# Kernel tuning notes

Measured on AMD Instinct MI355X. Metric: run time of the kernel, lower is better.

## Reference

```python
import jax, jax.numpy as jnp
import numpy as np

B, D, N = 2, 512, 2048
H, MQ, MV = 8, 64, 64
SCALE = 1.0 / np.sqrt(D).astype(np.float32)  # 1/sqrt(num_dim_q), full dim


def setup_inputs() -> dict:
    key = jax.random.key(0)
    ks = jax.random.split(key, 9)
    s = 0.02
    return {
        "Q": jax.random.normal(ks[0], (B, D, N), jnp.float32),
        "Wq": jax.random.normal(ks[1], (MQ * H, D), jnp.float32) * s,
        "bq": jnp.zeros((MQ * H,), jnp.float32),
        "Wk": jax.random.normal(ks[2], (MQ * H, D), jnp.float32) * s,
        "bk": jnp.zeros((MQ * H,), jnp.float32),
        "Wv": jax.random.normal(ks[3], (MV * H, D), jnp.float32) * s,
        "bv": jnp.zeros((MV * H,), jnp.float32),
        "Wo": jax.random.normal(ks[4], (D, MV * H), jnp.float32) * s,
        "bo": jnp.zeros((D,), jnp.float32),
    }


def _conv1x1(x, W, b):
    # Conv1d with kernel_size=1 == per-position linear: [B,Cin,N] -> [B,Cout,N]
    return jnp.einsum("bcn,oc->bon", x, W) + b[None, :, None]


def reference(Q, Wq, bq, Wk, bk, Wv, bv, Wo, bo):
    q = _conv1x1(Q, Wq, bq)  # [B, MQ*H, N]
    k = _conv1x1(Q, Wk, bk)
    v = _conv1x1(Q, Wv, bv)  # [B, MV*H, N]
    b = Q.shape[0]
    n = Q.shape[2]
    # channel index factors as (dim, head): channel = d*H + h (matches torch .view)
    q = q.reshape(b, MQ, H, n)
    k = k.reshape(b, MQ, H, n)
    v = v.reshape(b, MV, H, n)
    scores = jnp.einsum("bdhq,bdhk->bhqk", q, k) * SCALE  # [B,H,Nq,Nk]
    attn = jax.nn.softmax(scores, axis=-1)
    o = jnp.einsum("bhqk,bdhk->bdhq", attn, v)  # [B, MV, H, Nq]
    o = o.reshape(b, MV * H, n)
    return _conv1x1(o, Wo, bo)  # [B, D, N]
```

## Files before the change

kernel.cpp:

```cpp
#include <hip/hip_runtime.h>

#define DEV __device__ __forceinline__

typedef __bf16 bf16;
typedef __bf16 bf16x8 __attribute__((ext_vector_type(8)));
typedef __bf16 bf16x4 __attribute__((ext_vector_type(4)));
typedef float f32x4 __attribute__((ext_vector_type(4)));

#define B_ 2
#define D_ 512
#define N_ 2048
#define H_ 8
#define MD_ 64
#define SCALE_F (0.04419417382415922f * 1.4426950408889634f)

DEV void gload_lds16(const void* g, void* l) {
  __builtin_amdgcn_global_load_lds(
      (const __attribute__((address_space(1))) void*)g,
      (__attribute__((address_space(3))) void*)l, 16, 0, 0);
}

DEV f32x4 mfma16(bf16x8 a, bf16x8 b, f32x4 c) {
  return __builtin_amdgcn_mfma_f32_16x16x32_bf16(a, b, c, 0, 0, 0);
}

__global__ __launch_bounds__(256) void prep_w(
    const float* __restrict__ Wq, const float* __restrict__ bq,
    const float* __restrict__ Wk, const float* __restrict__ bk,
    const float* __restrict__ Wv, const float* __restrict__ bv,
    const float* __restrict__ Wo,
    bf16* __restrict__ Wf, float* __restrict__ biasf, bf16* __restrict__ Wor) {
  int row = blockIdx.x;
  int t = threadIdx.x;
  if (row < 1536) {
    const float* src;
    float scale = 1.0f;
    if (row < 512)       { src = Wq + (size_t)row * 512; scale = SCALE_F; }
    else if (row < 1024) { src = Wk + (size_t)(row - 512) * 512; }
    else                 { src = Wv + (size_t)(row - 1024) * 512; }
    for (int c = t; c < 512; c += 256)
      Wf[(size_t)row * 512 + c] = (bf16)(src[c] * scale);
    if (t == 0) {
      float bb;
      if (row < 512)       bb = bq[row] * SCALE_F;
      else if (row < 1024) bb = bk[row - 512];
      else                 bb = bv[row - 1024];
      biasf[row] = bb;
    }
  } else {
    int r = row - 1536;
    for (int c2 = t; c2 < 512; c2 += 256) {
      int hh = c2 >> 6, dd = c2 & 63;
      Wor[(size_t)r * 512 + c2] = (bf16)Wo[(size_t)r * 512 + dd * 8 + hh];
    }
  }
}

__global__ __launch_bounds__(256) void prep_qt(const float* __restrict__ Q,
                                               bf16* __restrict__ Qt) {
  __shared__ float tile[64][65];
  int b = blockIdx.z;
  int d0 = blockIdx.y * 64;
  int n0 = blockIdx.x * 64;
  int t = threadIdx.x;
  int r = t >> 2, cw = t & 3;

  const float* src = Q + ((size_t)(b * 512 + d0 + r)) * 2048 + n0 + cw * 16;
#pragma unroll
  for (int e4 = 0; e4 < 4; ++e4) {
    float4 v = *(const float4*)(src + e4 * 4);
    tile[r][cw * 16 + e4 * 4 + 0] = v.x;
    tile[r][cw * 16 + e4 * 4 + 1] = v.y;
    tile[r][cw * 16 + e4 * 4 + 2] = v.z;
    tile[r][cw * 16 + e4 * 4 + 3] = v.w;
  }
  __syncthreads();
  bf16x8 o0{}, o1{};
#pragma unroll
  for (int e = 0; e < 8; ++e) {
    o0[e] = (bf16)tile[cw * 16 + e][r];
    o1[e] = (bf16)tile[cw * 16 + 8 + e][r];
  }
  bf16* dst = Qt + ((size_t)(b * 2048 + n0 + r)) * 512 + d0 + cw * 16;
  *(bf16x8*)dst = o0;
  *((bf16x8*)dst + 1) = o1;
}

__global__ __launch_bounds__(256) void qkv_gemm(
    const bf16* __restrict__ Wf, const bf16* __restrict__ Qt,
    const float* __restrict__ biasf,
    bf16* __restrict__ qp, bf16* __restrict__ kp, bf16* __restrict__ vn) {
  __shared__ bf16 Al[128 * 32];
  __shared__ bf16 Bl[64 * 32];
  int b = blockIdx.z;
  int c0 = blockIdx.x * 128;
  int p0 = blockIdx.y * 64;
  int tid = threadIdx.x, w = tid >> 6, lane = tid & 63;
  int wm = w >> 1, wn = w & 1;
  int g = lane >> 4, l15 = lane & 15;

  const bf16* Abase = Wf + (size_t)c0 * 512;
  const bf16* Bbase = Qt + ((size_t)b * 2048 + p0) * 512;

  f32x4 acc[4][2] = {};

  for (int ks = 0; ks < 16; ++ks) {
    int k0 = ks * 32;
    __syncthreads();
#pragma unroll
    for (int i = 0; i < 2; ++i) {
      int rowl = w * 32 + i * 16 + (lane >> 2);
      gload_lds16(Abase + (size_t)rowl * 512 + k0 + (lane & 3) * 8,
                  Al + (w * 32 + i * 16) * 32);
    }
    {
      int browl = w * 16 + (lane >> 2);
      gload_lds16(Bbase + (size_t)browl * 512 + k0 + (lane & 3) * 8,
                  Bl + w * 16 * 32);
    }
    __syncthreads();
    bf16x8 a[4], bb[2];
#pragma unroll
    for (int mi = 0; mi < 4; ++mi)
      a[mi] = *(const bf16x8*)(Al + (wm * 64 + mi * 16 + l15) * 32 + g * 8);
#pragma unroll
    for (int ni = 0; ni < 2; ++ni)
      bb[ni] = *(const bf16x8*)(Bl + (wn * 32 + ni * 16 + l15) * 32 + g * 8);
#pragma unroll
    for (int mi = 0; mi < 4; ++mi)
#pragma unroll
      for (int ni = 0; ni < 2; ++ni)
        acc[mi][ni] = mfma16(a[mi], bb[ni], acc[mi][ni]);
  }

#pragma unroll
  for (int mi = 0; mi < 4; ++mi) {
#pragma unroll
    for (int ni = 0; ni < 2; ++ni) {
#pragma unroll
      for (int r = 0; r < 4; ++r) {
        int row = c0 + wm * 64 + mi * 16 + g * 4 + r;
        int p = p0 + wn * 32 + ni * 16 + l15;
        float val = acc[mi][ni][r] + biasf[row];
        bf16 hv = (bf16)val;
        if (row < 512) {
          int c = row;
          qp[(((size_t)b * 8 + (c & 7)) * 2048 + p) * 64 + (c >> 3)] = hv;
        } else if (row < 1024) {
          int c = row - 512;
          kp[(((size_t)b * 8 + (c & 7)) * 2048 + p) * 64 + (c >> 3)] = hv;
        } else {
          int c = row - 1024;
          vn[((size_t)b * 512 + c) * 2048 + p] = hv;
        }
      }
    }
  }
}

__global__ __launch_bounds__(512) void attn_k(
    const bf16* __restrict__ qp, const bf16* __restrict__ kp,
    const bf16* __restrict__ vn, bf16* __restrict__ Op,
    float* __restrict__ mbuf, float* __restrict__ lbuf) {
  __shared__ bf16 Ks[2][64 * 64];
  __shared__ bf16 Vs[2][64 * 64];
  __shared__ bf16 Ps[128 * 64];
  int q0 = blockIdx.x * 128;
  int bh = blockIdx.y;
  int z = blockIdx.z;
  int b = bh >> 3, h = bh & 7;
  int tid = threadIdx.x, w = tid >> 6, lane = tid & 63;
  int g = lane >> 4, l15 = lane & 15;
  int irow = w * 16 + l15;

  bf16x8 qreg[2];
#pragma unroll
  for (int ks2 = 0; ks2 < 2; ++ks2)
    qreg[ks2] = *(const bf16x8*)(qp + ((size_t)bh * 2048 + q0 + irow) * 64 +
                                 ks2 * 32 + g * 8);

  int krow = tid >> 3;
  int kch = (tid & 7) ^ (krow & 7);

  const bf16* Kall = kp + (size_t)bh * 2048 * 64 + (size_t)z * 16 * 64 * 64;
  const bf16* Vall = vn + ((size_t)(b * 512 + h)) * 2048 + (size_t)z * 16 * 64;

  gload_lds16(Kall + (size_t)krow * 64 + kch * 8, Ks[0] + w * 512);
  gload_lds16(Vall + (size_t)krow * 16384 + kch * 8, Vs[0] + w * 512);

  f32x4 oacc[4] = {};
  float mrow = -1e30f, rs = 0.0f;

  __syncthreads();

  for (int t = 0; t < 16; ++t) {
    int cur = t & 1, nxt = cur ^ 1;
    int tn = (t < 15) ? t + 1 : 15;

    gload_lds16(Kall + (size_t)tn * 64 * 64 + (size_t)krow * 64 + kch * 8,
                Ks[nxt] + w * 512);
    gload_lds16(Vall + (size_t)tn * 64 + (size_t)krow * 16384 + kch * 8,
                Vs[nxt] + w * 512);

    f32x4 st[4] = {};
    __builtin_amdgcn_s_setprio(1);
#pragma unroll
    for (int ks2 = 0; ks2 < 2; ++ks2) {
#pragma unroll
      for (int jt = 0; jt < 4; ++jt) {
        int jrow = jt * 16 + l15;
        bf16x8 kb = *(const bf16x8*)(Ks[cur] + jrow * 64 + (((ks2 * 4 + g) ^ (jrow & 7)) << 3));
        st[jt] = mfma16(kb, qreg[ks2], st[jt]);
      }
    }
    __builtin_amdgcn_s_setprio(0);

    float rm = st[0][0];
#pragma unroll
    for (int jt = 0; jt < 4; ++jt)
#pragma unroll
      for (int i = 0; i < 4; ++i) rm = fmaxf(rm, st[jt][i]);
    rm = fmaxf(rm, __shfl_xor(rm, 16));
    rm = fmaxf(rm, __shfl_xor(rm, 32));

    if (__any(rm > mrow + 8.0f)) {
      float nm = fmaxf(mrow, rm);
      float esc = __builtin_amdgcn_exp2f(mrow - nm);
      mrow = nm;
      rs *= esc;
#pragma unroll
      for (int r = 0; r < 4; ++r) {
        float er = __shfl(esc, g * 4 + r, 64);
#pragma unroll
        for (int dt = 0; dt < 4; ++dt) oacc[dt][r] *= er;
      }
    }

#pragma unroll
    for (int jt = 0; jt < 4; ++jt) {
      bf16x4 pk;
#pragma unroll
      for (int i = 0; i < 4; ++i) {
        float pv = __builtin_amdgcn_exp2f(st[jt][i] - mrow);
        rs += pv;
        pk[i] = (bf16)pv;
      }
      int j0 = jt * 16 + g * 4;
      *(bf16x4*)(Ps + irow * 64 + (j0 ^ ((irow & 7) << 3))) = pk;
    }

    __builtin_amdgcn_s_setprio(1);
#pragma unroll
    for (int ks2 = 0; ks2 < 2; ++ks2) {
      bf16x8 pa = *(const bf16x8*)(Ps + irow * 64 + (((ks2 * 4 + g) ^ (irow & 7)) << 3));
#pragma unroll
      for (int dt = 0; dt < 4; ++dt) {
        int drow = dt * 16 + l15;
        bf16x8 vb = *(const bf16x8*)(Vs[cur] + drow * 64 + (((ks2 * 4 + g) ^ (drow & 7)) << 3));
        oacc[dt] = mfma16(pa, vb, oacc[dt]);
      }
    }
    __builtin_amdgcn_s_setprio(0);

    __syncthreads();
  }

  rs += __shfl_xor(rs, 16);
  rs += __shfl_xor(rs, 32);

  size_t zoff = (size_t)z * 16 * 2048;
#pragma unroll
  for (int dt = 0; dt < 4; ++dt) {
#pragma unroll
    for (int r = 0; r < 4; ++r) {
      int i = w * 16 + g * 4 + r;
      Op[(zoff + (size_t)bh * 2048 + q0 + i) * 64 + dt * 16 + l15] =
          (bf16)oacc[dt][r];
    }
  }
  if (lane < 16) {
    mbuf[zoff + (size_t)bh * 2048 + q0 + w * 16 + l15] = mrow;
    lbuf[zoff + (size_t)bh * 2048 + q0 + w * 16 + l15] = rs;
  }
}

__global__ __launch_bounds__(256) void combine(
    const bf16* __restrict__ Op, const float* __restrict__ mbuf,
    const float* __restrict__ lbuf, bf16* __restrict__ oh) {
  int idx = blockIdx.x * 256 + threadIdx.x;
  int row = idx >> 2;
  int dc = (idx & 3) * 16;
  float m0 = mbuf[row], m1 = mbuf[32768 + row];
  float l0 = lbuf[row], l1 = lbuf[32768 + row];
  float M = fmaxf(m0, m1);
  float w0 = __builtin_amdgcn_exp2f(m0 - M);
  float w1 = __builtin_amdgcn_exp2f(m1 - M);
  float invL = 1.0f / (w0 * l0 + w1 * l1);
  float a0 = w0 * invL, a1 = w1 * invL;

  const bf16x8* p0 = (const bf16x8*)(Op + (size_t)row * 64 + dc);
  const bf16x8* p1 = (const bf16x8*)(Op + (size_t)32768 * 64 + (size_t)row * 64 + dc);
  bf16x8* po = (bf16x8*)(oh + (size_t)row * 64 + dc);
#pragma unroll
  for (int v = 0; v < 2; ++v) {
    bf16x8 x0 = p0[v], x1 = p1[v];
    bf16x8 o;
#pragma unroll
    for (int e = 0; e < 8; ++e)
      o[e] = (bf16)(a0 * (float)x0[e] + a1 * (float)x1[e]);
    po[v] = o;
  }
}

__global__ __launch_bounds__(256) void out_gemm(
    const bf16* __restrict__ Wor, const bf16* __restrict__ oh,
    const float* __restrict__ bo, float* __restrict__ out) {
  __shared__ bf16 Al[128 * 32];
  __shared__ bf16 Bl[64 * 32];
  int b = blockIdx.z;
  int r0 = blockIdx.x * 128;
  int p0 = blockIdx.y * 64;
  int tid = threadIdx.x, w = tid >> 6, lane = tid & 63;
  int wm = w >> 1, wn = w & 1;
  int g = lane >> 4, l15 = lane & 15;

  const bf16* Abase = Wor + (size_t)r0 * 512;

  f32x4 acc[4][2] = {};

  for (int ks = 0; ks < 16; ++ks) {
    int k0 = ks * 32;
    int hh = k0 >> 6, d0 = k0 & 63;
    const bf16* Bbase = oh + (((size_t)b * 8 + hh) * 2048 + p0) * 64 + d0;
    __syncthreads();
#pragma unroll
    for (int i = 0; i < 2; ++i) {
      int rowl = w * 32 + i * 16 + (lane >> 2);
      gload_lds16(Abase + (size_t)rowl * 512 + k0 + (lane & 3) * 8,
                  Al + (w * 32 + i * 16) * 32);
    }
    {
      int browl = w * 16 + (lane >> 2);
      gload_lds16(Bbase + (size_t)browl * 64 + (lane & 3) * 8,
                  Bl + w * 16 * 32);
    }
    __syncthreads();
    bf16x8 a[4], bb[2];
#pragma unroll
    for (int mi = 0; mi < 4; ++mi)
      a[mi] = *(const bf16x8*)(Al + (wm * 64 + mi * 16 + l15) * 32 + g * 8);
#pragma unroll
    for (int ni = 0; ni < 2; ++ni)
      bb[ni] = *(const bf16x8*)(Bl + (wn * 32 + ni * 16 + l15) * 32 + g * 8);
#pragma unroll
    for (int mi = 0; mi < 4; ++mi)
#pragma unroll
      for (int ni = 0; ni < 2; ++ni)
        acc[mi][ni] = mfma16(a[mi], bb[ni], acc[mi][ni]);
  }

#pragma unroll
  for (int mi = 0; mi < 4; ++mi) {
#pragma unroll
    for (int ni = 0; ni < 2; ++ni) {
#pragma unroll
      for (int r = 0; r < 4; ++r) {
        int row = r0 + wm * 64 + mi * 16 + g * 4 + r;
        int p = p0 + wn * 32 + ni * 16 + l15;
        out[((size_t)b * 512 + row) * 2048 + p] = acc[mi][ni][r] + bo[row];
      }
    }
  }
}

extern "C" void kernel_launch(void* const* d_in, const int* in_sizes, int n_in,
                              void* d_out, int out_size, void* d_ws, size_t ws_size,
                              hipStream_t stream) {
  (void)in_sizes; (void)n_in; (void)out_size; (void)ws_size;
  const float* Q  = (const float*)d_in[0];
  const float* Wq = (const float*)d_in[1];
  const float* bq = (const float*)d_in[2];
  const float* Wk = (const float*)d_in[3];
  const float* bk = (const float*)d_in[4];
  const float* Wv = (const float*)d_in[5];
  const float* bv = (const float*)d_in[6];
  const float* Wo = (const float*)d_in[7];
  const float* bo = (const float*)d_in[8];
  float* out = (float*)d_out;

  char* ws = (char*)d_ws;
  bf16*  Wf    = (bf16*)(ws + 0);
  bf16*  Wor   = (bf16*)(ws + 1572864);
  float* biasf = (float*)(ws + 2097152);
  bf16*  Qt    = (bf16*)(ws + 2103296);
  bf16*  qp    = (bf16*)(ws + 6297600);
  bf16*  kp    = (bf16*)(ws + 10491904);
  bf16*  vn    = (bf16*)(ws + 14686208);
  bf16*  oh    = (bf16*)(ws + 18880512);
  bf16*  Opart = (bf16*)(ws + 23074816);
  float* mbuf  = (float*)(ws + 31463424);
  float* lbuf  = (float*)(ws + 31725568);

  prep_w<<<dim3(2048), dim3(256), 0, stream>>>(Wq, bq, Wk, bk, Wv, bv, Wo,
                                               Wf, biasf, Wor);
  prep_qt<<<dim3(32, 8, 2), dim3(256), 0, stream>>>(Q, Qt);
  qkv_gemm<<<dim3(12, 32, 2), dim3(256), 0, stream>>>(Wf, Qt, biasf, qp, kp, vn);
  attn_k<<<dim3(16, 16, 2), dim3(512), 0, stream>>>(qp, kp, vn, Opart, mbuf, lbuf);
  combine<<<dim3(512), dim3(256), 0, stream>>>(Opart, mbuf, lbuf, oh);
  out_gemm<<<dim3(4, 32, 2), dim3(256), 0, stream>>>(Wor, oh, bo, out);
}
```

Baseline: 81.92 us.

## Double-buffer GEMM LDS tiles and give each attention wave two query row groups

The QKV and output projection GEMMs now keep two LDS buffers. The next K-slice is issued before the MFMAs on the current slice, which removes one barrier per iteration and overlaps global loads with compute. The attention kernel drops from 512 to 256 threads, and each wave handles 32 query rows as two 16-row groups. Each K/V fragment read from LDS is then reused for two MFMAs, at the cost of more registers per thread and half as many waves per block. LDS use per GEMM block doubles.

```diff
diff --git a/kernel.cpp b/kernel.cpp
--- a/kernel.cpp
+++ b/kernel.cpp
@@ -90,8 +90,8 @@
     const bf16* __restrict__ Wf, const bf16* __restrict__ Qt,
     const float* __restrict__ biasf,
     bf16* __restrict__ qp, bf16* __restrict__ kp, bf16* __restrict__ vn) {
-  __shared__ bf16 Al[128 * 32];
-  __shared__ bf16 Bl[64 * 32];
+  __shared__ bf16 Al[2][128 * 32];
+  __shared__ bf16 Bl[2][64 * 32];
   int b = blockIdx.z;
   int c0 = blockIdx.x * 128;
   int p0 = blockIdx.y * 64;
@@ -102,35 +102,43 @@
   const bf16* Abase = Wf + (size_t)c0 * 512;
   const bf16* Bbase = Qt + ((size_t)b * 2048 + p0) * 512;
 
+  int arow0 = lane >> 2;
+  int ach = lane & 3;
+
   f32x4 acc[4][2] = {};
 
+#pragma unroll
+  for (int i = 0; i < 2; ++i)
+    gload_lds16(Abase + (size_t)(w * 32 + i * 16 + arow0) * 512 + ach * 8,
+                Al[0] + (w * 32 + i * 16) * 32);
+  gload_lds16(Bbase + (size_t)(w * 16 + arow0) * 512 + ach * 8,
+              Bl[0] + w * 16 * 32);
+  __syncthreads();
+
   for (int ks = 0; ks < 16; ++ks) {
-    int k0 = ks * 32;
-    __syncthreads();
-#pragma unroll
-    for (int i = 0; i < 2; ++i) {
-      int rowl = w * 32 + i * 16 + (lane >> 2);
-      gload_lds16(Abase + (size_t)rowl * 512 + k0 + (lane & 3) * 8,
-                  Al + (w * 32 + i * 16) * 32);
-    }
-    {
-      int browl = w * 16 + (lane >> 2);
-      gload_lds16(Bbase + (size_t)browl * 512 + k0 + (lane & 3) * 8,
-                  Bl + w * 16 * 32);
-    }
-    __syncthreads();
+    int cur = ks & 1, nxt = cur ^ 1;
+    if (ks < 15) {
+      int k0 = (ks + 1) * 32;
+#pragma unroll
+      for (int i = 0; i < 2; ++i)
+        gload_lds16(Abase + (size_t)(w * 32 + i * 16 + arow0) * 512 + k0 + ach * 8,
+                    Al[nxt] + (w * 32 + i * 16) * 32);
+      gload_lds16(Bbase + (size_t)(w * 16 + arow0) * 512 + k0 + ach * 8,
+                  Bl[nxt] + w * 16 * 32);
+    }
     bf16x8 a[4], bb[2];
 #pragma unroll
     for (int mi = 0; mi < 4; ++mi)
-      a[mi] = *(const bf16x8*)(Al + (wm * 64 + mi * 16 + l15) * 32 + g * 8);
+      a[mi] = *(const bf16x8*)(Al[cur] + (wm * 64 + mi * 16 + l15) * 32 + g * 8);
 #pragma unroll
     for (int ni = 0; ni < 2; ++ni)
-      bb[ni] = *(const bf16x8*)(Bl + (wn * 32 + ni * 16 + l15) * 32 + g * 8);
+      bb[ni] = *(const bf16x8*)(Bl[cur] + (wn * 32 + ni * 16 + l15) * 32 + g * 8);
 #pragma unroll
     for (int mi = 0; mi < 4; ++mi)
 #pragma unroll
       for (int ni = 0; ni < 2; ++ni)
         acc[mi][ni] = mfma16(a[mi], bb[ni], acc[mi][ni]);
+    __syncthreads();
   }
 
 #pragma unroll
@@ -158,7 +166,7 @@
   }
 }
 
-__global__ __launch_bounds__(512) void attn_k(
+__global__ __launch_bounds__(256) void attn_k(
     const bf16* __restrict__ qp, const bf16* __restrict__ kp,
     const bf16* __restrict__ vn, bf16* __restrict__ Op,
     float* __restrict__ mbuf, float* __restrict__ lbuf) {
@@ -171,25 +179,32 @@
   int b = bh >> 3, h = bh & 7;
   int tid = threadIdx.x, w = tid >> 6, lane = tid & 63;
   int g = lane >> 4, l15 = lane & 15;
-  int irow = w * 16 + l15;
-
-  bf16x8 qreg[2];
-#pragma unroll
-  for (int ks2 = 0; ks2 < 2; ++ks2)
-    qreg[ks2] = *(const bf16x8*)(qp + ((size_t)bh * 2048 + q0 + irow) * 64 +
-                                 ks2 * 32 + g * 8);
+
+  bf16x8 qreg[2][2];
+#pragma unroll
+  for (int rg = 0; rg < 2; ++rg)
+#pragma unroll
+    for (int ks2 = 0; ks2 < 2; ++ks2)
+      qreg[rg][ks2] = *(const bf16x8*)(
+          qp + ((size_t)bh * 2048 + q0 + w * 32 + rg * 16 + l15) * 64 +
+          ks2 * 32 + g * 8);
 
   int krow = tid >> 3;
-  int kch = (tid & 7) ^ (krow & 7);
+  int kch = tid & 7;
 
   const bf16* Kall = kp + (size_t)bh * 2048 * 64 + (size_t)z * 16 * 64 * 64;
   const bf16* Vall = vn + ((size_t)(b * 512 + h)) * 2048 + (size_t)z * 16 * 64;
 
-  gload_lds16(Kall + (size_t)krow * 64 + kch * 8, Ks[0] + w * 512);
-  gload_lds16(Vall + (size_t)krow * 16384 + kch * 8, Vs[0] + w * 512);
-
-  f32x4 oacc[4] = {};
-  float mrow = -1e30f, rs = 0.0f;
+#pragma unroll
+  for (int i = 0; i < 2; ++i) {
+    int row = krow + i * 32;
+    int ch = kch ^ (row & 7);
+    gload_lds16(Kall + (size_t)row * 64 + ch * 8, Ks[0] + (w * 8 + i * 32) * 64);
+    gload_lds16(Vall + (size_t)row * 16384 + ch * 8, Vs[0] + (w * 8 + i * 32) * 64);
+  }
+
+  f32x4 oacc[2][4] = {};
+  float mrow[2] = {-1e30f, -1e30f}, rs[2] = {0.0f, 0.0f};
 
   __syncthreads();
 
@@ -197,67 +212,92 @@
     int cur = t & 1, nxt = cur ^ 1;
     int tn = (t < 15) ? t + 1 : 15;
 
-    gload_lds16(Kall + (size_t)tn * 64 * 64 + (size_t)krow * 64 + kch * 8,
-                Ks[nxt] + w * 512);
-    gload_lds16(Vall + (size_t)tn * 64 + (size_t)krow * 16384 + kch * 8,
-                Vs[nxt] + w * 512);
-
-    f32x4 st[4] = {};
+#pragma unroll
+    for (int i = 0; i < 2; ++i) {
+      int row = krow + i * 32;
+      int ch = kch ^ (row & 7);
+      gload_lds16(Kall + (size_t)tn * 4096 + (size_t)row * 64 + ch * 8,
+                  Ks[nxt] + (w * 8 + i * 32) * 64);
+      gload_lds16(Vall + (size_t)tn * 64 + (size_t)row * 16384 + ch * 8,
+                  Vs[nxt] + (w * 8 + i * 32) * 64);
+    }
+
+    f32x4 st[2][4] = {};
     __builtin_amdgcn_s_setprio(1);
 #pragma unroll
     for (int ks2 = 0; ks2 < 2; ++ks2) {
 #pragma unroll
       for (int jt = 0; jt < 4; ++jt) {
         int jrow = jt * 16 + l15;
-        bf16x8 kb = *(const bf16x8*)(Ks[cur] + jrow * 64 + (((ks2 * 4 + g) ^ (jrow & 7)) << 3));
-        st[jt] = mfma16(kb, qreg[ks2], st[jt]);
+        bf16x8 kb = *(const bf16x8*)(Ks[cur] + jrow * 64 +
+                                     (((ks2 * 4 + g) ^ (jrow & 7)) << 3));
+        st[0][jt] = mfma16(kb, qreg[0][ks2], st[0][jt]);
+        st[1][jt] = mfma16(kb, qreg[1][ks2], st[1][jt]);
       }
     }
     __builtin_amdgcn_s_setprio(0);
 
-    float rm = st[0][0];
-#pragma unroll
-    for (int jt = 0; jt < 4; ++jt)
-#pragma unroll
-      for (int i = 0; i < 4; ++i) rm = fmaxf(rm, st[jt][i]);
-    rm = fmaxf(rm, __shfl_xor(rm, 16));
-    rm = fmaxf(rm, __shfl_xor(rm, 32));
-
-    if (__any(rm > mrow + 8.0f)) {
-      float nm = fmaxf(mrow, rm);
-      float esc = __builtin_amdgcn_exp2f(mrow - nm);
-      mrow = nm;
-      rs *= esc;
-#pragma unroll
-      for (int r = 0; r < 4; ++r) {
-        float er = __shfl(esc, g * 4 + r, 64);
-#pragma unroll
-        for (int dt = 0; dt < 4; ++dt) oacc[dt][r] *= er;
-      }
-    }
-
-#pragma unroll
-    for (int jt = 0; jt < 4; ++jt) {
-      bf16x4 pk;
-#pragma unroll
-      for (int i = 0; i < 4; ++i) {
-        float pv = __builtin_amdgcn_exp2f(st[jt][i] - mrow);
-        rs += pv;
-        pk[i] = (bf16)pv;
-      }
-      int j0 = jt * 16 + g * 4;
-      *(bf16x4*)(Ps + irow * 64 + (j0 ^ ((irow & 7) << 3))) = pk;
+    float rm[2];
+#pragma unroll
+    for (int rg = 0; rg < 2; ++rg) {
+      float m0 = st[rg][0][0];
+#pragma unroll
+      for (int jt = 0; jt < 4; ++jt)
+#pragma unroll
+        for (int i = 0; i < 4; ++i) m0 = fmaxf(m0, st[rg][jt][i]);
+      m0 = fmaxf(m0, __shfl_xor(m0, 16));
+      m0 = fmaxf(m0, __shfl_xor(m0, 32));
+      rm[rg] = m0;
+    }
+
+    if (__any(fmaxf(rm[0] - mrow[0], rm[1] - mrow[1]) > 8.0f)) {
+#pragma unroll
+      for (int rg = 0; rg < 2; ++rg) {
+        float nm = fmaxf(mrow[rg], rm[rg]);
+        float esc = __builtin_amdgcn_exp2f(mrow[rg] - nm);
+        mrow[rg] = nm;
+        rs[rg] *= esc;
+#pragma unroll
+        for (int r = 0; r < 4; ++r) {
+          float er = __shfl(esc, g * 4 + r, 64);
+#pragma unroll
+          for (int dt = 0; dt < 4; ++dt) oacc[rg][dt][r] *= er;
+        }
+      }
+    }
+
+#pragma unroll
+    for (int rg = 0; rg < 2; ++rg) {
+      int prow = w * 32 + rg * 16 + l15;
+#pragma unroll
+      for (int jt = 0; jt < 4; ++jt) {
+        bf16x4 pk;
+#pragma unroll
+        for (int i = 0; i < 4; ++i) {
+          float pv = __builtin_amdgcn_exp2f(st[rg][jt][i] - mrow[rg]);
+          rs[rg] += pv;
+          pk[i] = (bf16)pv;
+        }
+        *(bf16x4*)(Ps + prow * 64 + ((jt * 16 + g * 4) ^ ((prow & 7) << 3))) = pk;
+      }
     }
 
     __builtin_amdgcn_s_setprio(1);
 #pragma unroll
     for (int ks2 = 0; ks2 < 2; ++ks2) {
-      bf16x8 pa = *(const bf16x8*)(Ps + irow * 64 + (((ks2 * 4 + g) ^ (irow & 7)) << 3));
+      int r0w = w * 32 + l15;
+      int r1w = w * 32 + 16 + l15;
+      bf16x8 pa0 = *(const bf16x8*)(Ps + r0w * 64 +
+                                    (((ks2 * 4 + g) ^ (r0w & 7)) << 3));
+      bf16x8 pa1 = *(const bf16x8*)(Ps + r1w * 64 +
+                                    (((ks2 * 4 + g) ^ (r1w & 7)) << 3));
 #pragma unroll
       for (int dt = 0; dt < 4; ++dt) {
         int drow = dt * 16 + l15;
-        bf16x8 vb = *(const bf16x8*)(Vs[cur] + drow * 64 + (((ks2 * 4 + g) ^ (drow & 7)) << 3));
-        oacc[dt] = mfma16(pa, vb, oacc[dt]);
+        bf16x8 vb = *(const bf16x8*)(Vs[cur] + drow * 64 +
+                                     (((ks2 * 4 + g) ^ (drow & 7)) << 3));
+        oacc[0][dt] = mfma16(pa0, vb, oacc[0][dt]);
+        oacc[1][dt] = mfma16(pa1, vb, oacc[1][dt]);
       }
     }
     __builtin_amdgcn_s_setprio(0);
@@ -265,22 +305,32 @@
     __syncthreads();
   }
 
-  rs += __shfl_xor(rs, 16);
-  rs += __shfl_xor(rs, 32);
+#pragma unroll
+  for (int rg = 0; rg < 2; ++rg) {
+    rs[rg] += __shfl_xor(rs[rg], 16);
+    rs[rg] += __shfl_xor(rs[rg], 32);
+  }
 
   size_t zoff = (size_t)z * 16 * 2048;
 #pragma unroll
-  for (int dt = 0; dt < 4; ++dt) {
-#pragma unroll
-    for (int r = 0; r < 4; ++r) {
-      int i = w * 16 + g * 4 + r;
-      Op[(zoff + (size_t)bh * 2048 + q0 + i) * 64 + dt * 16 + l15] =
-          (bf16)oacc[dt][r];
+  for (int rg = 0; rg < 2; ++rg) {
+#pragma unroll
+    for (int dt = 0; dt < 4; ++dt) {
+#pragma unroll
+      for (int r = 0; r < 4; ++r) {
+        int i = w * 32 + rg * 16 + g * 4 + r;
+        Op[(zoff + (size_t)bh * 2048 + q0 + i) * 64 + dt * 16 + l15] =
+            (bf16)oacc[rg][dt][r];
+      }
     }
   }
   if (lane < 16) {
-    mbuf[zoff + (size_t)bh * 2048 + q0 + w * 16 + l15] = mrow;
-    lbuf[zoff + (size_t)bh * 2048 + q0 + w * 16 + l15] = rs;
+#pragma unroll
+    for (int rg = 0; rg < 2; ++rg) {
+      int i = w * 32 + rg * 16 + l15;
+      mbuf[zoff + (size_t)bh * 2048 + q0 + i] = mrow[rg];
+      lbuf[zoff + (size_t)bh * 2048 + q0 + i] = rs[rg];
+    }
   }
 }
 
@@ -315,8 +365,8 @@
 __global__ __launch_bounds__(256) void out_gemm(
     const bf16* __restrict__ Wor, const bf16* __restrict__ oh,
     const float* __restrict__ bo, float* __restrict__ out) {
-  __shared__ bf16 Al[128 * 32];
-  __shared__ bf16 Bl[64 * 32];
+  __shared__ bf16 Al[2][128 * 32];
+  __shared__ bf16 Bl[2][64 * 32];
   int b = blockIdx.z;
   int r0 = blockIdx.x * 128;
   int p0 = blockIdx.y * 64;
@@ -325,38 +375,46 @@
   int g = lane >> 4, l15 = lane & 15;
 
   const bf16* Abase = Wor + (size_t)r0 * 512;
+  const bf16* Bhead = oh + (size_t)b * 8 * 2048 * 64 + (size_t)p0 * 64;
+
+  int arow0 = lane >> 2;
+  int ach = lane & 3;
 
   f32x4 acc[4][2] = {};
 
+#pragma unroll
+  for (int i = 0; i < 2; ++i)
+    gload_lds16(Abase + (size_t)(w * 32 + i * 16 + arow0) * 512 + ach * 8,
+                Al[0] + (w * 32 + i * 16) * 32);
+  gload_lds16(Bhead + (size_t)(w * 16 + arow0) * 64 + ach * 8,
+              Bl[0] + w * 16 * 32);
+  __syncthreads();
+
   for (int ks = 0; ks < 16; ++ks) {
-    int k0 = ks * 32;
-    int hh = k0 >> 6, d0 = k0 & 63;
-    const bf16* Bbase = oh + (((size_t)b * 8 + hh) * 2048 + p0) * 64 + d0;
-    __syncthreads();
-#pragma unroll
-    for (int i = 0; i < 2; ++i) {
-      int rowl = w * 32 + i * 16 + (lane >> 2);
-      gload_lds16(Abase + (size_t)rowl * 512 + k0 + (lane & 3) * 8,
-                  Al + (w * 32 + i * 16) * 32);
-    }
-    {
-      int browl = w * 16 + (lane >> 2);
-      gload_lds16(Bbase + (size_t)browl * 64 + (lane & 3) * 8,
-                  Bl + w * 16 * 32);
-    }
-    __syncthreads();
+    int cur = ks & 1, nxt = cur ^ 1;
+    if (ks < 15) {
+      int k0 = (ks + 1) * 32;
+      const bf16* Bbase = Bhead + (size_t)(k0 >> 6) * 2048 * 64 + (k0 & 63);
+#pragma unroll
+      for (int i = 0; i < 2; ++i)
+        gload_lds16(Abase + (size_t)(w * 32 + i * 16 + arow0) * 512 + k0 + ach * 8,
+                    Al[nxt] + (w * 32 + i * 16) * 32);
+      gload_lds16(Bbase + (size_t)(w * 16 + arow0) * 64 + ach * 8,
+                  Bl[nxt] + w * 16 * 32);
+    }
     bf16x8 a[4], bb[2];
 #pragma unroll
     for (int mi = 0; mi < 4; ++mi)
-      a[mi] = *(const bf16x8*)(Al + (wm * 64 + mi * 16 + l15) * 32 + g * 8);
+      a[mi] = *(const bf16x8*)(Al[cur] + (wm * 64 + mi * 16 + l15) * 32 + g * 8);
 #pragma unroll
     for (int ni = 0; ni < 2; ++ni)
-      bb[ni] = *(const bf16x8*)(Bl + (wn * 32 + ni * 16 + l15) * 32 + g * 8);
+      bb[ni] = *(const bf16x8*)(Bl[cur] + (wn * 32 + ni * 16 + l15) * 32 + g * 8);
 #pragma unroll
     for (int mi = 0; mi < 4; ++mi)
 #pragma unroll
       for (int ni = 0; ni < 2; ++ni)
         acc[mi][ni] = mfma16(a[mi], bb[ni], acc[mi][ni]);
+    __syncthreads();
   }
 
 #pragma unroll
@@ -405,7 +463,7 @@
                                                Wf, biasf, Wor);
   prep_qt<<<dim3(32, 8, 2), dim3(256), 0, stream>>>(Q, Qt);
   qkv_gemm<<<dim3(12, 32, 2), dim3(256), 0, stream>>>(Wf, Qt, biasf, qp, kp, vn);
-  attn_k<<<dim3(16, 16, 2), dim3(512), 0, stream>>>(qp, kp, vn, Opart, mbuf, lbuf);
+  attn_k<<<dim3(16, 16, 2), dim3(256), 0, stream>>>(qp, kp, vn, Opart, mbuf, lbuf);
   combine<<<dim3(512), dim3(256), 0, stream>>>(Opart, mbuf, lbuf, oh);
   out_gemm<<<dim3(4, 32, 2), dim3(256), 0, stream>>>(Wor, oh, bo, out);
 }
```

New measurement: 87.80 us. 7.2% more time.
